# Optimization experiments

Measured on AMD Instinct MI355X. Metric: run time of the kernel, lower is better.

The kernel has to match this reference:

```python
import jax, jax.numpy as jnp
import numpy as np

B, F, H, T = 2048, 128, 512, 96  # batch, n_features, hidden_size, output_length


def setup_inputs() -> dict:
    key = jax.random.key(0)
    ks = jax.random.split(key, 7)
    s_ih = 1.0 / np.sqrt(H)
    return {
        "hidden": jax.random.normal(ks[0], (B, H), dtype=jnp.float32),
        "w_ih": jax.random.uniform(ks[1], (3 * H, F), jnp.float32, -s_ih, s_ih),
        "w_hh": jax.random.uniform(ks[2], (3 * H, H), jnp.float32, -s_ih, s_ih),
        "b_ih": jax.random.uniform(ks[3], (3 * H,), jnp.float32, -s_ih, s_ih),
        "b_hh": jax.random.uniform(ks[4], (3 * H,), jnp.float32, -s_ih, s_ih),
        "fc_w": jax.random.uniform(ks[5], (F, H), jnp.float32, -s_ih, s_ih),
        "fc_b": jax.random.uniform(ks[6], (F,), jnp.float32, -s_ih, s_ih),
    }


def reference(hidden, w_ih, w_hh, b_ih, b_hh, fc_w, fc_b):
    x0 = jnp.zeros((hidden.shape[0], F), dtype=hidden.dtype)  # initial_input=None

    def step(carry, _):
        h, x = carry
        gi = x @ w_ih.T + b_ih            # [B, 3H]
        gh = h @ w_hh.T + b_hh            # [B, 3H]
        i_r, i_z, i_n = jnp.split(gi, 3, axis=-1)
        h_r, h_z, h_n = jnp.split(gh, 3, axis=-1)
        r = jax.nn.sigmoid(i_r + h_r)
        z = jax.nn.sigmoid(i_z + h_z)
        n = jnp.tanh(i_n + r * h_n)
        h_new = (1.0 - z) * n + z * h
        x_new = h_new @ fc_w.T + fc_b     # [B, F]
        return (h_new, x_new), x_new

    _, ys = jax.lax.scan(step, (hidden, x0), None, length=T)  # [T, B, F]
    out = jnp.transpose(ys, (1, 0, 2))     # [B, T, F]
    out = out[:, ::-1, :]                  # backwards=True: outputs.insert(0, ...)
    return out
```

## Files before the change

kernel.cpp:

```cpp
#include <hip/hip_runtime.h>
#include <hip/hip_bf16.h>

#define HH 512
#define FF 128
#define BB 2048
#define TT 96
#define NSTEP 96
#define NGATE 2048
#define NTOT 2176
#define GRP 16
#define CPB 32

typedef short short8 __attribute__((ext_vector_type(8)));
typedef float f32x4 __attribute__((ext_vector_type(4)));

__device__ __forceinline__ float sigmoidf_(float x) { return 1.f / (1.f + __expf(-x)); }
__device__ __forceinline__ float tanhf_(float x) {
    float e = __expf(-2.f * fabsf(x));
    float t = (1.f - e) / (1.f + e);
    return x < 0.f ? -t : t;
}

__device__ __forceinline__ size_t frag_off(int m, int k, int K) {
    return (size_t)((m >> 4) * (K >> 5) + (k >> 5)) * 1024
         + (size_t)(((k >> 3) & 3) * 256 + (m & 15) * 16 + (k & 7) * 2);
}

__device__ __forceinline__ short bf16bits(float f) {
    __hip_bfloat16 b = __float2bfloat16(f);
    return *(short*)&b;
}

__global__ __launch_bounds__(256) void build_weights(
    const float* __restrict__ w_ih, const float* __restrict__ w_hh,
    const float* __restrict__ b_ih, const float* __restrict__ b_hh,
    const float* __restrict__ fc_w, const float* __restrict__ fc_b,
    char* __restrict__ Wg, char* __restrict__ W0g, char* __restrict__ Wfc,
    float* __restrict__ bias, float* __restrict__ bias0)
{
    const int n = blockIdx.x;
    const int tid = threadIdx.x;
    __shared__ float wih_s[FF];
    const bool is_out = (n >= NGATE);
    int gate = 3, gidx = 0, f = 0;
    if (is_out) {
        f = n - NGATE;
    } else {
        int j = (n >> 4) * 4 + ((n >> 2) & 3);
        gate = n & 3;
        gidx = (gate == 0) ? j : (gate == 1) ? (512 + j) : (1024 + j);
    }
    if (!is_out && gate != 3 && tid < FF) wih_s[tid] = w_ih[gidx * FF + tid];
    __syncthreads();

    for (int k = tid; k < HH; k += 256) {
        float w, w0;
        if (is_out) {
            w = fc_w[f * HH + k];
            w0 = 0.f;
        } else if (gate == 3) {
            w = w_hh[gidx * HH + k];
            w0 = w;
        } else {
            float comb = 0.f;
#pragma unroll 8
            for (int ff2 = 0; ff2 < FF; ++ff2) comb += wih_s[ff2] * fc_w[ff2 * HH + k];
            if (gate == 2) { w = comb; w0 = 0.f; }
            else { float whh = w_hh[gidx * HH + k]; w = whh + comb; w0 = whh; }
        }
        if (is_out) {
            *(short*)(Wfc + frag_off(f, k, HH)) = bf16bits(w);
        } else {
            *(short*)(Wg  + frag_off(n, k, HH)) = bf16bits(w);
            *(short*)(W0g + frag_off(n, k, HH)) = bf16bits(w0);
        }
    }
    if (tid == 0 && !is_out) {
        float b, b0;
        float cb = 0.f;
        if (gate != 3)
            for (int ff2 = 0; ff2 < FF; ++ff2) cb += fc_b[ff2] * w_ih[gidx * FF + ff2];
        if (gate <= 1)      { float s2 = b_ih[gidx] + b_hh[gidx]; b = s2 + cb; b0 = s2; }
        else if (gate == 2) { b = b_ih[gidx] + cb; b0 = b_ih[gidx]; }
        else                { b = b_hh[gidx]; b0 = b_hh[gidx]; }
        bias[n] = b; bias0[n] = b0;
    }
}

__global__ __launch_bounds__(256) void init_misc(
    const float* __restrict__ hidden, char* __restrict__ hfrag, int* __restrict__ cnt)
{
    int i = blockIdx.x * 256 + threadIdx.x;
    int row = i >> 6, k0 = (i & 63) << 3;
    short8 v;
#pragma unroll
    for (int t = 0; t < 8; ++t) v[t] = bf16bits(hidden[(size_t)row * HH + k0 + t]);
    *(short8*)(hfrag + frag_off(row, k0, HH)) = v;
    if (i < GRP * NSTEP * CPB) cnt[i] = 0;
}

__global__ __launch_bounds__(256, 2) void gru_persist(
    const char* __restrict__ Wg, const char* __restrict__ W0g, const char* __restrict__ Wfc,
    const float* __restrict__ bias, const float* __restrict__ bias0,
    const float* __restrict__ fc_b, const float* __restrict__ hidden,
    char* __restrict__ hfrag0, char* __restrict__ hfrag1,
    float* __restrict__ out, int* __restrict__ cnt)
{
    __shared__ __align__(16) short Bs[32768];
    __shared__ __align__(16) short hfr[2048];

    const int tid = threadIdx.x;
    const int lane = tid & 63, w = tid >> 6;
    const int l15 = lane & 15, quad = lane >> 4;
    const int g = blockIdx.x & 15, c = blockIdx.x >> 4;

    const char* aB0 = hfrag0 + (size_t)(g * 8 + w * 2) * 16384 + lane * 16;
    const char* aB1 = hfrag1 + (size_t)(g * 8 + w * 2) * 16384 + lane * 16;
    const char* bf  = Wfc + (size_t)(c & 7) * 16384 + lane * 16;
    const char* wlds = (const char*)Bs + lane * 16;
    const int fcq = c >> 3;

    f32x4 bv4[4];
#pragma unroll
    for (int mt = 0; mt < 4; ++mt)
        bv4[mt] = *(const f32x4*)&bias[c * 64 + mt * 16 + quad * 4];
    const f32x4 fcb4 = *(const f32x4*)&fc_b[(c & 7) * 16 + quad * 4];

    float carry[4][2];
#pragma unroll
    for (int mt = 0; mt < 4; ++mt)
#pragma unroll
        for (int btl = 0; btl < 2; ++btl)
            carry[mt][btl] =
                hidden[(size_t)(g * 128 + w * 32 + btl * 16 + l15) * HH
                       + c * 16 + mt * 4 + quad];

    int* const fl = cnt + g * (NSTEP * CPB);

    {
        const char* wsrc = Wg + (size_t)c * 65536;
#pragma unroll
        for (int i = 0; i < 16; ++i) {
            int idx = i * 256 + tid;
            *(int4*)((char*)Bs + idx * 16) = *(const int4*)(wsrc + (size_t)idx * 16);
        }
    }
    __syncthreads();

    auto grp_wait = [&](int s) {
        if (w == 0) {
            if (lane < 32) {
                const int* fp = fl + s * CPB + lane;
                while (__hip_atomic_load(fp, __ATOMIC_RELAXED, __HIP_MEMORY_SCOPE_AGENT) == 0)
                    __builtin_amdgcn_s_sleep(1);
            }
            asm volatile("buffer_inv sc0\n\ts_waitcnt vmcnt(0)" ::: "memory");
        }
        __syncthreads();
        asm volatile("" ::: "memory");
    };

    auto epilogue = [&](f32x4 (&acc)[4][2], int s, char* hout) {
#pragma unroll
        for (int mt = 0; mt < 4; ++mt)
#pragma unroll
            for (int btl = 0; btl < 2; ++btl) {
                f32x4 a = acc[mt][btl];
                float r  = sigmoidf_(a[0]);
                float z  = sigmoidf_(a[1]);
                float nv = tanhf_(a[2] + r * a[3]);
                float hn = (1.f - z) * nv + z * carry[mt][btl];
                carry[mt][btl] = hn;
                hfr[(w * 32 + btl * 16 + l15) * 16 + mt * 4 + quad] = bf16bits(hn);
            }
        __syncthreads();
        {
            int lrow = tid >> 1, half = tid & 1;
            size_t off = (size_t)((g * 8 + (lrow >> 4)) * 16 + (c >> 1)) * 1024
                       + (size_t)((((c << 1) + half) & 3) * 256 + (lrow & 15) * 16);
            *(int4*)(hout + off) = *(const int4*)&hfr[lrow * 16 + half * 8];
        }
        asm volatile("s_waitcnt vmcnt(0)" ::: "memory");
        __syncthreads();
        if (tid == 0)
            __hip_atomic_store(fl + s * CPB + c, 1, __ATOMIC_RELAXED, __HIP_MEMORY_SCOPE_AGENT);
    };

    {
        f32x4 acc[4][2];
#pragma unroll
        for (int mt = 0; mt < 4; ++mt) {
            f32x4 b0 = *(const f32x4*)&bias0[c * 64 + mt * 16 + quad * 4];
            acc[mt][0] = b0; acc[mt][1] = b0;
        }
        const char* w0b = W0g + (size_t)c * 65536 + lane * 16;
        short8 W0[2][4]; short8 Hb[2][2];
#pragma unroll
        for (int p = 0; p < 2; ++p) {
#pragma unroll
            for (int mt = 0; mt < 4; ++mt)
                W0[p][mt] = *(const short8*)(w0b + (size_t)(mt * 16 + p) * 1024);
#pragma unroll
            for (int btl = 0; btl < 2; ++btl)
                Hb[p][btl] = *(const short8*)(aB0 + btl * 16384 + p * 1024);
        }
#pragma unroll
        for (int it = 0; it < 16; ++it) {
            const int sl = it & 1;
#pragma unroll
            for (int mt = 0; mt < 4; ++mt)
#pragma unroll
                for (int btl = 0; btl < 2; ++btl)
                    acc[mt][btl] = __builtin_amdgcn_mfma_f32_16x16x32_bf16(W0[sl][mt], Hb[sl][btl], acc[mt][btl], 0, 0, 0);
            if (it + 2 < 16) {
#pragma unroll
                for (int mt = 0; mt < 4; ++mt)
                    W0[sl][mt] = *(const short8*)(w0b + (size_t)(mt * 16 + it + 2) * 1024);
#pragma unroll
                for (int btl = 0; btl < 2; ++btl)
                    Hb[sl][btl] = *(const short8*)(aB0 + btl * 16384 + (it + 2) * 1024);
            }
        }
        epilogue(acc, 0, hfrag1);
    }

    for (int s = 1; s < 96; ++s) {
        const char* ab = (s & 1) ? aB1 : aB0;
        char* hout = (s & 1) ? hfrag0 : hfrag1;
        const bool dofc = ((s & 3) == fcq);

        f32x4 acc[4][2];
#pragma unroll
        for (int mt = 0; mt < 4; ++mt) {
            acc[mt][0] = bv4[mt]; acc[mt][1] = bv4[mt];
        }
        f32x4 fca[2] = {{0.f,0.f,0.f,0.f},{0.f,0.f,0.f,0.f}};

        short8 Wa[2][4]; short8 Wf[2];
#pragma unroll
        for (int p = 0; p < 2; ++p)
#pragma unroll
            for (int mt = 0; mt < 4; ++mt)
                Wa[p][mt] = *(const short8*)(wlds + (size_t)(mt * 16 + p) * 1024);
        if (dofc) {
            Wf[0] = *(const short8*)(bf);
            Wf[1] = *(const short8*)(bf + 1024);
        }

        grp_wait(s - 1);

        short8 Hb[6][2];
#pragma unroll
        for (int p = 0; p < 6; ++p)
#pragma unroll
            for (int btl = 0; btl < 2; ++btl)
                Hb[p][btl] = *(const short8*)(ab + btl * 16384 + p * 1024);

#pragma unroll
        for (int it = 0; it < 16; ++it) {
            const int sa = it % 6, sw = it & 1;
#pragma unroll
            for (int mt = 0; mt < 4; ++mt)
#pragma unroll
                for (int btl = 0; btl < 2; ++btl)
                    acc[mt][btl] = __builtin_amdgcn_mfma_f32_16x16x32_bf16(Wa[sw][mt], Hb[sa][btl], acc[mt][btl], 0, 0, 0);
            if (dofc) {
                fca[0] = __builtin_amdgcn_mfma_f32_16x16x32_bf16(Wf[sw], Hb[sa][0], fca[0], 0, 0, 0);
                fca[1] = __builtin_amdgcn_mfma_f32_16x16x32_bf16(Wf[sw], Hb[sa][1], fca[1], 0, 0, 0);
            }
            if (it + 6 < 16) {
#pragma unroll
                for (int btl = 0; btl < 2; ++btl)
                    Hb[sa][btl] = *(const short8*)(ab + btl * 16384 + (it + 6) * 1024);
            }
            if (it + 2 < 16) {
#pragma unroll
                for (int mt = 0; mt < 4; ++mt)
                    Wa[sw][mt] = *(const short8*)(wlds + (size_t)(mt * 16 + it + 2) * 1024);
                if (dofc) Wf[sw] = *(const short8*)(bf + (size_t)(it + 2) * 1024);
            }
        }

        if (dofc) {
            const int tt = 96 - s;
#pragma unroll
            for (int btl = 0; btl < 2; ++btl) {
                f32x4 v = fca[btl] + fcb4;
                *(f32x4*)&out[(size_t)(g * 128 + w * 32 + btl * 16 + l15) * (TT * FF)
                              + tt * FF + (c & 7) * 16 + quad * 4] = v;
            }
        }

        epilogue(acc, s, hout);
    }

    if (fcq == 0) {
        grp_wait(95);
        f32x4 fca[2] = {{0.f,0.f,0.f,0.f},{0.f,0.f,0.f,0.f}};
        short8 Wf[2]; short8 Hb[2][2];
#pragma unroll
        for (int p = 0; p < 2; ++p) {
            Wf[p] = *(const short8*)(bf + (size_t)p * 1024);
#pragma unroll
            for (int btl = 0; btl < 2; ++btl)
                Hb[p][btl] = *(const short8*)(aB0 + btl * 16384 + p * 1024);
        }
#pragma unroll
        for (int it = 0; it < 16; ++it) {
            const int sl = it & 1;
            fca[0] = __builtin_amdgcn_mfma_f32_16x16x32_bf16(Wf[sl], Hb[sl][0], fca[0], 0, 0, 0);
            fca[1] = __builtin_amdgcn_mfma_f32_16x16x32_bf16(Wf[sl], Hb[sl][1], fca[1], 0, 0, 0);
            if (it + 2 < 16) {
                Wf[sl] = *(const short8*)(bf + (size_t)(it + 2) * 1024);
#pragma unroll
                for (int btl = 0; btl < 2; ++btl)
                    Hb[sl][btl] = *(const short8*)(aB0 + btl * 16384 + (it + 2) * 1024);
            }
        }
#pragma unroll
        for (int btl = 0; btl < 2; ++btl) {
            f32x4 v = fca[btl] + fcb4;
            *(f32x4*)&out[(size_t)(g * 128 + w * 32 + btl * 16 + l15) * (TT * FF)
                          + (c & 7) * 16 + quad * 4] = v;
        }
    }
}

extern "C" void kernel_launch(void* const* d_in, const int* in_sizes, int n_in,
                              void* d_out, int out_size, void* d_ws, size_t ws_size,
                              hipStream_t stream) {
    const float* hidden = (const float*)d_in[0];
    const float* w_ih   = (const float*)d_in[1];
    const float* w_hh   = (const float*)d_in[2];
    const float* b_ih   = (const float*)d_in[3];
    const float* b_hh   = (const float*)d_in[4];
    const float* fc_w   = (const float*)d_in[5];
    const float* fc_b   = (const float*)d_in[6];
    float* out = (float*)d_out;

    char* ws = (char*)d_ws;
    size_t off = 0;
    auto alloc = [&](size_t bytes) -> void* {
        void* p = ws + off;
        off += (bytes + 255) & ~(size_t)255;
        return p;
    };
    char* Wg   = (char*)alloc((size_t)NGATE * HH * 2);
    char* W0g  = (char*)alloc((size_t)NGATE * HH * 2);
    char* Wfc  = (char*)alloc((size_t)FF * HH * 2);
    float* bias  = (float*)alloc(NGATE * 4);
    float* bias0 = (float*)alloc(NGATE * 4);
    char* hfrag0 = (char*)alloc((size_t)BB * HH * 2);
    char* hfrag1 = (char*)alloc((size_t)BB * HH * 2);
    int* cnt = (int*)alloc((size_t)GRP * NSTEP * CPB * 4);

    build_weights<<<NTOT, 256, 0, stream>>>(w_ih, w_hh, b_ih, b_hh, fc_w, fc_b,
                                            Wg, W0g, Wfc, bias, bias0);
    init_misc<<<(BB * HH / 8 + 255) / 256, 256, 0, stream>>>(hidden, hfrag0, cnt);
    gru_persist<<<512, 256, 0, stream>>>(Wg, W0g, Wfc, bias, bias0, fc_b, hidden,
                                         hfrag0, hfrag1, out, cnt);
}
```

Before: 809.6 us.

## Split gate tiles across two waves per row block, doubling block size

Each block now runs 8 waves instead of 4. Paired waves split the four gate m-tiles of a row block, so each wave does half the MFMAs and keeps half the accumulators. The aim is to shorten the per-step critical path of the serial recurrence by spreading each step's work over more waves. The H-fragment prefetch depth drops from 6 to 4 to save registers, and the FC work stays on only the even waves. The cost is that both waves of a pair load the same H fragments, and the larger block may change occupancy under the new 512-thread launch bounds.

```diff
diff --git a/kernel.cpp b/kernel.cpp
--- a/kernel.cpp
+++ b/kernel.cpp
@@ -99,7 +99,7 @@
     if (i < GRP * NSTEP * CPB) cnt[i] = 0;
 }
 
-__global__ __launch_bounds__(256, 2) void gru_persist(
+__global__ __launch_bounds__(512, 4) void gru_persist(
     const char* __restrict__ Wg, const char* __restrict__ W0g, const char* __restrict__ Wfc,
     const float* __restrict__ bias, const float* __restrict__ bias0,
     const float* __restrict__ fc_b, const float* __restrict__ hidden,
@@ -112,36 +112,39 @@
     const int tid = threadIdx.x;
     const int lane = tid & 63, w = tid >> 6;
     const int l15 = lane & 15, quad = lane >> 4;
+    const int mhalf = w & 1;
+    const int wrow = w >> 1;
     const int g = blockIdx.x & 15, c = blockIdx.x >> 4;
 
-    const char* aB0 = hfrag0 + (size_t)(g * 8 + w * 2) * 16384 + lane * 16;
-    const char* aB1 = hfrag1 + (size_t)(g * 8 + w * 2) * 16384 + lane * 16;
+    const char* aB0 = hfrag0 + (size_t)(g * 8 + wrow * 2) * 16384 + lane * 16;
+    const char* aB1 = hfrag1 + (size_t)(g * 8 + wrow * 2) * 16384 + lane * 16;
     const char* bf  = Wfc + (size_t)(c & 7) * 16384 + lane * 16;
     const char* wlds = (const char*)Bs + lane * 16;
     const int fcq = c >> 3;
-
-    f32x4 bv4[4];
-#pragma unroll
-    for (int mt = 0; mt < 4; ++mt)
-        bv4[mt] = *(const f32x4*)&bias[c * 64 + mt * 16 + quad * 4];
+    const bool fcw = (mhalf == 0);
+
+    f32x4 bv4[2];
+#pragma unroll
+    for (int mt = 0; mt < 2; ++mt)
+        bv4[mt] = *(const f32x4*)&bias[c * 64 + (mhalf * 2 + mt) * 16 + quad * 4];
     const f32x4 fcb4 = *(const f32x4*)&fc_b[(c & 7) * 16 + quad * 4];
 
-    float carry[4][2];
-#pragma unroll
-    for (int mt = 0; mt < 4; ++mt)
+    float carry[2][2];
+#pragma unroll
+    for (int mt = 0; mt < 2; ++mt)
 #pragma unroll
         for (int btl = 0; btl < 2; ++btl)
             carry[mt][btl] =
-                hidden[(size_t)(g * 128 + w * 32 + btl * 16 + l15) * HH
-                       + c * 16 + mt * 4 + quad];
+                hidden[(size_t)(g * 128 + wrow * 32 + btl * 16 + l15) * HH
+                       + c * 16 + mhalf * 8 + mt * 4 + quad];
 
     int* const fl = cnt + g * (NSTEP * CPB);
 
     {
         const char* wsrc = Wg + (size_t)c * 65536;
 #pragma unroll
-        for (int i = 0; i < 16; ++i) {
-            int idx = i * 256 + tid;
+        for (int i = 0; i < 8; ++i) {
+            int idx = i * 512 + tid;
             *(int4*)((char*)Bs + idx * 16) = *(const int4*)(wsrc + (size_t)idx * 16);
         }
     }
@@ -160,9 +163,9 @@
         asm volatile("" ::: "memory");
     };
 
-    auto epilogue = [&](f32x4 (&acc)[4][2], int s, char* hout) {
-#pragma unroll
-        for (int mt = 0; mt < 4; ++mt)
+    auto epilogue = [&](f32x4 (&acc)[2][2], int s, char* hout) {
+#pragma unroll
+        for (int mt = 0; mt < 2; ++mt)
 #pragma unroll
             for (int btl = 0; btl < 2; ++btl) {
                 f32x4 a = acc[mt][btl];
@@ -171,10 +174,10 @@
                 float nv = tanhf_(a[2] + r * a[3]);
                 float hn = (1.f - z) * nv + z * carry[mt][btl];
                 carry[mt][btl] = hn;
-                hfr[(w * 32 + btl * 16 + l15) * 16 + mt * 4 + quad] = bf16bits(hn);
+                hfr[(wrow * 32 + btl * 16 + l15) * 16 + mhalf * 8 + mt * 4 + quad] = bf16bits(hn);
             }
         __syncthreads();
-        {
+        if (tid < 256) {
             int lrow = tid >> 1, half = tid & 1;
             size_t off = (size_t)((g * 8 + (lrow >> 4)) * 16 + (c >> 1)) * 1024
                        + (size_t)((((c << 1) + half) & 3) * 256 + (lrow & 15) * 16);
@@ -187,19 +190,19 @@
     };
 
     {
-        f32x4 acc[4][2];
-#pragma unroll
-        for (int mt = 0; mt < 4; ++mt) {
-            f32x4 b0 = *(const f32x4*)&bias0[c * 64 + mt * 16 + quad * 4];
+        f32x4 acc[2][2];
+#pragma unroll
+        for (int mt = 0; mt < 2; ++mt) {
+            f32x4 b0 = *(const f32x4*)&bias0[c * 64 + (mhalf * 2 + mt) * 16 + quad * 4];
             acc[mt][0] = b0; acc[mt][1] = b0;
         }
         const char* w0b = W0g + (size_t)c * 65536 + lane * 16;
-        short8 W0[2][4]; short8 Hb[2][2];
+        short8 W0[2][2]; short8 Hb[2][2];
 #pragma unroll
         for (int p = 0; p < 2; ++p) {
 #pragma unroll
-            for (int mt = 0; mt < 4; ++mt)
-                W0[p][mt] = *(const short8*)(w0b + (size_t)(mt * 16 + p) * 1024);
+            for (int mt = 0; mt < 2; ++mt)
+                W0[p][mt] = *(const short8*)(w0b + (size_t)((mhalf * 2 + mt) * 16 + p) * 1024);
 #pragma unroll
             for (int btl = 0; btl < 2; ++btl)
                 Hb[p][btl] = *(const short8*)(aB0 + btl * 16384 + p * 1024);
@@ -208,14 +211,14 @@
         for (int it = 0; it < 16; ++it) {
             const int sl = it & 1;
 #pragma unroll
-            for (int mt = 0; mt < 4; ++mt)
+            for (int mt = 0; mt < 2; ++mt)
 #pragma unroll
                 for (int btl = 0; btl < 2; ++btl)
                     acc[mt][btl] = __builtin_amdgcn_mfma_f32_16x16x32_bf16(W0[sl][mt], Hb[sl][btl], acc[mt][btl], 0, 0, 0);
             if (it + 2 < 16) {
 #pragma unroll
-                for (int mt = 0; mt < 4; ++mt)
-                    W0[sl][mt] = *(const short8*)(w0b + (size_t)(mt * 16 + it + 2) * 1024);
+                for (int mt = 0; mt < 2; ++mt)
+                    W0[sl][mt] = *(const short8*)(w0b + (size_t)((mhalf * 2 + mt) * 16 + it + 2) * 1024);
 #pragma unroll
                 for (int btl = 0; btl < 2; ++btl)
                     Hb[sl][btl] = *(const short8*)(aB0 + btl * 16384 + (it + 2) * 1024);
@@ -227,21 +230,21 @@
     for (int s = 1; s < 96; ++s) {
         const char* ab = (s & 1) ? aB1 : aB0;
         char* hout = (s & 1) ? hfrag0 : hfrag1;
-        const bool dofc = ((s & 3) == fcq);
-
-        f32x4 acc[4][2];
-#pragma unroll
-        for (int mt = 0; mt < 4; ++mt) {
+        const bool dofc = fcw && ((s & 3) == fcq);
+
+        f32x4 acc[2][2];
+#pragma unroll
+        for (int mt = 0; mt < 2; ++mt) {
             acc[mt][0] = bv4[mt]; acc[mt][1] = bv4[mt];
         }
         f32x4 fca[2] = {{0.f,0.f,0.f,0.f},{0.f,0.f,0.f,0.f}};
 
-        short8 Wa[2][4]; short8 Wf[2];
+        short8 Wa[2][2]; short8 Wf[2];
 #pragma unroll
         for (int p = 0; p < 2; ++p)
 #pragma unroll
-            for (int mt = 0; mt < 4; ++mt)
-                Wa[p][mt] = *(const short8*)(wlds + (size_t)(mt * 16 + p) * 1024);
+            for (int mt = 0; mt < 2; ++mt)
+                Wa[p][mt] = *(const short8*)(wlds + (size_t)((mhalf * 2 + mt) * 16 + p) * 1024);
         if (dofc) {
             Wf[0] = *(const short8*)(bf);
             Wf[1] = *(const short8*)(bf + 1024);
@@ -249,18 +252,18 @@
 
         grp_wait(s - 1);
 
-        short8 Hb[6][2];
-#pragma unroll
-        for (int p = 0; p < 6; ++p)
+        short8 Hb[4][2];
+#pragma unroll
+        for (int p = 0; p < 4; ++p)
 #pragma unroll
             for (int btl = 0; btl < 2; ++btl)
                 Hb[p][btl] = *(const short8*)(ab + btl * 16384 + p * 1024);
 
 #pragma unroll
         for (int it = 0; it < 16; ++it) {
-            const int sa = it % 6, sw = it & 1;
-#pragma unroll
-            for (int mt = 0; mt < 4; ++mt)
+            const int sa = it & 3, sw = it & 1;
+#pragma unroll
+            for (int mt = 0; mt < 2; ++mt)
 #pragma unroll
                 for (int btl = 0; btl < 2; ++btl)
                     acc[mt][btl] = __builtin_amdgcn_mfma_f32_16x16x32_bf16(Wa[sw][mt], Hb[sa][btl], acc[mt][btl], 0, 0, 0);
@@ -268,15 +271,15 @@
                 fca[0] = __builtin_amdgcn_mfma_f32_16x16x32_bf16(Wf[sw], Hb[sa][0], fca[0], 0, 0, 0);
                 fca[1] = __builtin_amdgcn_mfma_f32_16x16x32_bf16(Wf[sw], Hb[sa][1], fca[1], 0, 0, 0);
             }
-            if (it + 6 < 16) {
-#pragma unroll
-                for (int btl = 0; btl < 2; ++btl)
-                    Hb[sa][btl] = *(const short8*)(ab + btl * 16384 + (it + 6) * 1024);
+            if (it + 4 < 16) {
+#pragma unroll
+                for (int btl = 0; btl < 2; ++btl)
+                    Hb[sa][btl] = *(const short8*)(ab + btl * 16384 + (it + 4) * 1024);
             }
             if (it + 2 < 16) {
 #pragma unroll
-                for (int mt = 0; mt < 4; ++mt)
-                    Wa[sw][mt] = *(const short8*)(wlds + (size_t)(mt * 16 + it + 2) * 1024);
+                for (int mt = 0; mt < 2; ++mt)
+                    Wa[sw][mt] = *(const short8*)(wlds + (size_t)((mhalf * 2 + mt) * 16 + it + 2) * 1024);
                 if (dofc) Wf[sw] = *(const short8*)(bf + (size_t)(it + 2) * 1024);
             }
         }
@@ -286,7 +289,7 @@
 #pragma unroll
             for (int btl = 0; btl < 2; ++btl) {
                 f32x4 v = fca[btl] + fcb4;
-                *(f32x4*)&out[(size_t)(g * 128 + w * 32 + btl * 16 + l15) * (TT * FF)
+                *(f32x4*)&out[(size_t)(g * 128 + wrow * 32 + btl * 16 + l15) * (TT * FF)
                               + tt * FF + (c & 7) * 16 + quad * 4] = v;
             }
         }
@@ -296,32 +299,34 @@
 
     if (fcq == 0) {
         grp_wait(95);
-        f32x4 fca[2] = {{0.f,0.f,0.f,0.f},{0.f,0.f,0.f,0.f}};
-        short8 Wf[2]; short8 Hb[2][2];
-#pragma unroll
-        for (int p = 0; p < 2; ++p) {
-            Wf[p] = *(const short8*)(bf + (size_t)p * 1024);
-#pragma unroll
-            for (int btl = 0; btl < 2; ++btl)
-                Hb[p][btl] = *(const short8*)(aB0 + btl * 16384 + p * 1024);
-        }
-#pragma unroll
-        for (int it = 0; it < 16; ++it) {
-            const int sl = it & 1;
-            fca[0] = __builtin_amdgcn_mfma_f32_16x16x32_bf16(Wf[sl], Hb[sl][0], fca[0], 0, 0, 0);
-            fca[1] = __builtin_amdgcn_mfma_f32_16x16x32_bf16(Wf[sl], Hb[sl][1], fca[1], 0, 0, 0);
-            if (it + 2 < 16) {
-                Wf[sl] = *(const short8*)(bf + (size_t)(it + 2) * 1024);
-#pragma unroll
-                for (int btl = 0; btl < 2; ++btl)
-                    Hb[sl][btl] = *(const short8*)(aB0 + btl * 16384 + (it + 2) * 1024);
-            }
-        }
-#pragma unroll
-        for (int btl = 0; btl < 2; ++btl) {
-            f32x4 v = fca[btl] + fcb4;
-            *(f32x4*)&out[(size_t)(g * 128 + w * 32 + btl * 16 + l15) * (TT * FF)
-                          + (c & 7) * 16 + quad * 4] = v;
+        if (fcw) {
+            f32x4 fca[2] = {{0.f,0.f,0.f,0.f},{0.f,0.f,0.f,0.f}};
+            short8 Wf[2]; short8 Hb[2][2];
+#pragma unroll
+            for (int p = 0; p < 2; ++p) {
+                Wf[p] = *(const short8*)(bf + (size_t)p * 1024);
+#pragma unroll
+                for (int btl = 0; btl < 2; ++btl)
+                    Hb[p][btl] = *(const short8*)(aB0 + btl * 16384 + p * 1024);
+            }
+#pragma unroll
+            for (int it = 0; it < 16; ++it) {
+                const int sl = it & 1;
+                fca[0] = __builtin_amdgcn_mfma_f32_16x16x32_bf16(Wf[sl], Hb[sl][0], fca[0], 0, 0, 0);
+                fca[1] = __builtin_amdgcn_mfma_f32_16x16x32_bf16(Wf[sl], Hb[sl][1], fca[1], 0, 0, 0);
+                if (it + 2 < 16) {
+                    Wf[sl] = *(const short8*)(bf + (size_t)(it + 2) * 1024);
+#pragma unroll
+                    for (int btl = 0; btl < 2; ++btl)
+                        Hb[sl][btl] = *(const short8*)(aB0 + btl * 16384 + (it + 2) * 1024);
+                }
+            }
+#pragma unroll
+            for (int btl = 0; btl < 2; ++btl) {
+                f32x4 v = fca[btl] + fcb4;
+                *(f32x4*)&out[(size_t)(g * 128 + wrow * 32 + btl * 16 + l15) * (TT * FF)
+                              + (c & 7) * 16 + quad * 4] = v;
+            }
         }
     }
 }
@@ -357,6 +362,6 @@
     build_weights<<<NTOT, 256, 0, stream>>>(w_ih, w_hh, b_ih, b_hh, fc_w, fc_b,
                                             Wg, W0g, Wfc, bias, bias0);
     init_misc<<<(BB * HH / 8 + 255) / 256, 256, 0, stream>>>(hidden, hfrag0, cnt);
-    gru_persist<<<512, 256, 0, stream>>>(Wg, W0g, Wfc, bias, bias0, fc_b, hidden,
+    gru_persist<<<512, 512, 0, stream>>>(Wg, W0g, Wfc, bias, bias0, fc_b, hidden,
                                          hfrag0, hfrag1, out, cnt);
 }
```

Result: slower. 1.141 ms (+41.0%).
